# Kernel optimization log

Measured on AMD Instinct MI355X. Metric: run time of the kernel, lower is better.

## Reference

```python
import jax, jax.numpy as jnp
import numpy as np

EPS = 1e-5


def conv2d(x, w, b, stride=1, pad=1):
    out = jax.lax.conv_general_dilated(
        x, w, (stride, stride), [(pad, pad), (pad, pad)],
        dimension_numbers=('NCHW', 'OIHW', 'NCHW'))
    return out + b[None, :, None, None]


def bn_inf(x, gamma, beta, mean, var):
    inv = gamma / jnp.sqrt(var + EPS)
    return x * inv[None, :, None, None] + (beta - mean * inv)[None, :, None, None]


def deform_conv(x, offset, weight, stride, pad, dil):
    # x: [B,Ci,H,W], offset: [B,2*K*K,Ho,Wo] (dy,dx interleaved per kernel pos),
    # weight: [Co,Ci,K,K]. torchvision DeformConv2d v1 semantics, no bias.
    B, Ci, H, W = x.shape
    Co, _, K, _ = weight.shape
    KK = K * K
    Ho = (H + 2 * pad - dil * (K - 1) - 1) // stride + 1
    Wo = (W + 2 * pad - dil * (K - 1) - 1) // stride + 1
    dy = offset[:, 0::2]  # [B,KK,Ho,Wo]
    dx = offset[:, 1::2]
    ky, kx = jnp.meshgrid(jnp.arange(K), jnp.arange(K), indexing='ij')
    ky = ky.reshape(KK).astype(x.dtype)
    kx = kx.reshape(KK).astype(x.dtype)
    base_y = (jnp.arange(Ho) * stride - pad).astype(x.dtype)
    base_x = (jnp.arange(Wo) * stride - pad).astype(x.dtype)
    ys = base_y[None, None, :, None] + (ky * dil)[None, :, None, None] + dy
    xs = base_x[None, None, None, :] + (kx * dil)[None, :, None, None] + dx
    y0 = jnp.floor(ys)
    x0 = jnp.floor(xs)
    fy = ys - y0
    fx = xs - x0

    def gather(img, iy, ix):
        # img: [Ci,H,W]; iy, ix: [KK,Ho,Wo] float integer-valued coords
        valid = (iy >= 0) & (iy < H) & (ix >= 0) & (ix < W)
        iyc = jnp.clip(iy, 0, H - 1).astype(jnp.int32)
        ixc = jnp.clip(ix, 0, W - 1).astype(jnp.int32)
        v = img[:, iyc, ixc]  # [Ci,KK,Ho,Wo]
        return v * valid[None].astype(img.dtype)

    def sample_one(img, y0b, x0b, fyb, fxb):
        w00 = (1 - fyb) * (1 - fxb)
        w01 = (1 - fyb) * fxb
        w10 = fyb * (1 - fxb)
        w11 = fyb * fxb
        s = (gather(img, y0b, x0b) * w00[None]
             + gather(img, y0b, x0b + 1) * w01[None]
             + gather(img, y0b + 1, x0b) * w10[None]
             + gather(img, y0b + 1, x0b + 1) * w11[None])
        return s  # [Ci,KK,Ho,Wo]

    sampled = jax.vmap(sample_one)(x, y0, x0, fy, fx)  # [B,Ci,KK,Ho,Wo]
    return jnp.einsum('oik,bikhw->bohw', weight.reshape(Co, Ci, KK), sampled)


def setup_inputs() -> dict:
    key = jax.random.key(0)
    ks = jax.random.split(key, 16)
    B, C, H, W = 8, 128, 64, 64
    d = dict(
        x=jax.random.normal(ks[0], (B, C, H, W), jnp.float32),
        w_off1=jax.random.normal(ks[1], (18, C, 3, 3), jnp.float32) * 0.01,
        b_off1=jnp.zeros((18,), jnp.float32),
        w_dc1=jax.random.normal(ks[2], (C, C, 3, 3), jnp.float32) * 0.05,
        g1=jnp.ones((C,), jnp.float32),
        beta1=jnp.zeros((C,), jnp.float32),
        m1=jax.random.normal(ks[3], (C,), jnp.float32) * 0.1,
        v1=jax.random.uniform(ks[4], (C,), jnp.float32) + 0.5,
        w_off2=jax.random.normal(ks[5], (18, C, 3, 3), jnp.float32) * 0.01,
        b_off2=jnp.zeros((18,), jnp.float32),
        w_dc2=jax.random.normal(ks[6], (C, C, 3, 3), jnp.float32) * 0.05,
        g2=jnp.ones((C,), jnp.float32),
        beta2=jnp.zeros((C,), jnp.float32),
        m2=jax.random.normal(ks[7], (C,), jnp.float32) * 0.1,
        v2=jax.random.uniform(ks[8], (C,), jnp.float32) + 0.5,
    )
    return d


def reference(x, w_off1, b_off1, w_dc1, g1, beta1, m1, v1,
              w_off2, b_off2, w_dc2, g2, beta2, m2, v2):
    # BasicBlock6 forward (stride=1, in_planes==planes => identity shortcut)
    off1 = conv2d(x, w_off1, b_off1, stride=1, pad=1)
    out = jax.nn.relu(bn_inf(deform_conv(x, off1, w_dc1, 1, 2, 2), g1, beta1, m1, v1))
    off2 = conv2d(out, w_off2, b_off2, stride=1, pad=1)
    out = bn_inf(deform_conv(out, off2, w_dc2, 1, 2, 2), g2, beta2, m2, v2)
    out = out + x  # identity shortcut
    return jax.nn.relu(out)
```

## Files before the change

kernel.cpp:

```cpp
#include <hip/hip_runtime.h>
#include <hip/hip_bf16.h>

#define CH   128
#define HH   64
#define WW   64
#define OFFC 18

typedef __attribute__((ext_vector_type(8))) short bf16x8;
typedef __attribute__((ext_vector_type(4))) short bf16x4;
typedef __attribute__((ext_vector_type(4))) float f32x4;

static __device__ __forceinline__ unsigned short f2bf(float f) {
    __hip_bfloat16 h = __float2bfloat16(f);
    return *reinterpret_cast<unsigned short*>(&h);
}
static __device__ __forceinline__ float bf2f(unsigned short u) {
    union { unsigned int i; float f; } x; x.i = ((unsigned int)u) << 16;
    return x.f;
}

__global__ __launch_bounds__(256) void prep_kernel(
    const float* __restrict__ x, unsigned short* __restrict__ xh,
    const float* __restrict__ wdc1, const float* __restrict__ wdc2,
    const float* __restrict__ wof1, const float* __restrict__ wof2,
    unsigned short* __restrict__ wpk1, unsigned short* __restrict__ wpk2,
    unsigned short* __restrict__ wpo1, unsigned short* __restrict__ wpo2)
{
    __shared__ float s[CH][WW + 1];
    int blk = blockIdx.x;
    int tid = threadIdx.x;

    if (blk < 1152) {
        const float* w = (blk < 576) ? wdc1 : wdc2;
        unsigned short* wp = (blk < 576) ? wpk1 : wpk2;
        int id = (blk % 576) * 256 + tid;
        int j    = id & 7;
        int lane = (id >> 3) & 63;
        int ot   = (id >> 9) & 7;
        int kk   = (id >> 12) & 3;
        int k    = id >> 14;
        int o = ot * 16 + (lane & 15);
        int i = kk * 32 + (lane >> 4) * 8 + j;
        wp[id] = f2bf(w[(o * CH + i) * 9 + k]);
        return;
    }
    if (blk < 1440) {
        const float* w = (blk < 1296) ? wof1 : wof2;
        unsigned short* wp = (blk < 1296) ? wpo1 : wpo2;
        int id = ((blk - 1152) % 144) * 256 + tid;
        int j    = id & 7;
        int lane = (id >> 3) & 63;
        int mt   = (id >> 9) & 1;
        int kk   = (id >> 10) & 3;
        int k    = id >> 12;
        int o = mt * 16 + (lane & 15);
        int i = kk * 32 + (lane >> 4) * 8 + j;
        wp[id] = (o < OFFC) ? f2bf(w[(o * CH + i) * 9 + k]) : (unsigned short)0;
        return;
    }

    int nb = blk - 1440;
    const float* xb = x + ((size_t)(nb >> 6) * CH * HH + (nb & 63)) * WW;

    int c_off = tid >> 4, w0 = (tid & 15) * 4;
    #pragma unroll
    for (int it = 0; it < 8; ++it) {
        int c = it * 16 + c_off;
        float4 vv = *(const float4*)&xb[(size_t)c * HH * WW + w0];
        s[c][w0] = vv.x; s[c][w0 + 1] = vv.y; s[c][w0 + 2] = vv.z; s[c][w0 + 3] = vv.w;
    }
    __syncthreads();

    int w = tid & 63, c0 = (tid >> 6) * 32;
    unsigned short* dst = xh + ((size_t)nb * WW + w) * CH + c0;
    unsigned short tmp[32];
    #pragma unroll
    for (int j = 0; j < 32; ++j) tmp[j] = f2bf(s[c0 + j][w]);
    #pragma unroll
    for (int q = 0; q < 4; ++q)
        *(bf16x8*)(dst + q * 8) = *(const bf16x8*)(tmp + q * 8);
}

__global__ __launch_bounds__(256) void off_conv_mfma_kernel(
    const unsigned short* __restrict__ xh,
    const unsigned short* __restrict__ wpo,
    const float* __restrict__ bias,
    unsigned short* __restrict__ offh)
{
    int wgid = blockIdx.x;
    int blk  = (wgid & 7) * 64 + (wgid >> 3);
    int b = blk >> 6, oh = blk & 63;
    int tid = threadIdx.x;
    int lane = tid & 63;
    int nt = tid >> 6;
    int nl = lane & 15;
    int kg = lane >> 4;

    f32x4 acc0 = {0.f, 0.f, 0.f, 0.f}, acc1 = {0.f, 0.f, 0.f, 0.f};
    const unsigned short* xb = xh + (size_t)b * HH * WW * CH;

    for (int k = 0; k < 9; ++k) {
        int ky = k / 3, kx = k - ky * 3;
        int ih = oh - 1 + ky;
        if (ih < 0 || ih >= HH) continue;
        int iw = nt * 16 + nl + kx - 1;
        bool valid = (iw >= 0) && (iw < WW);
        const unsigned short* row = xb + ((size_t)ih * WW + (valid ? iw : 0)) * CH + kg * 8;
        const unsigned short* wk = wpo + (size_t)k * 8 * 512;
        #pragma unroll
        for (int kk = 0; kk < 4; ++kk) {
            bf16x8 bfrag = {0, 0, 0, 0, 0, 0, 0, 0};
            if (valid) bfrag = *(const bf16x8*)(row + kk * 32);
            bf16x8 a0 = *(const bf16x8*)(wk + (kk * 2 + 0) * 512 + lane * 8);
            bf16x8 a1 = *(const bf16x8*)(wk + (kk * 2 + 1) * 512 + lane * 8);
            acc0 = __builtin_amdgcn_mfma_f32_16x16x32_bf16(a0, bfrag, acc0, 0, 0, 0);
            acc1 = __builtin_amdgcn_mfma_f32_16x16x32_bf16(a1, bfrag, acc1, 0, 0, 0);
        }
    }

    int ow = nt * 16 + nl;
    #pragma unroll
    for (int r = 0; r < 4; ++r) {
        int co = kg * 4 + r;
        offh[(((size_t)b * OFFC + co) * HH + oh) * WW + ow] = f2bf(acc0[r] + bias[co]);
    }
    if (kg == 0) {
        #pragma unroll
        for (int r = 0; r < 2; ++r) {
            int co = 16 + r;
            offh[(((size_t)b * OFFC + co) * HH + oh) * WW + ow] = f2bf(acc1[r] + bias[co]);
        }
    }
}

#define DEF_COORD(K) do {                                                     \
    int ky = (K) / 3, kx = (K) - ky * 3;                                      \
    float ys = (float)(oh - 2 + ky * 2) + dyv[K];                             \
    float xs = (float)(ow_g - 2 + kx * 2) + dxv[K];                           \
    float y0f = floorf(ys), x0f = floorf(xs);                                 \
    float fy = ys - y0f, fx = xs - x0f;                                       \
    int y0 = (int)y0f, x0i = (int)x0f;                                        \
    int y1 = y0 + 1, x1 = x0i + 1;                                            \
    bool vy0 = (y0 >= 0) & (y0 < HH), vy1 = (y1 >= 0) & (y1 < HH);            \
    bool vx0 = (x0i >= 0) & (x0i < WW), vx1 = (x1 >= 0) & (x1 < WW);          \
    int y0c = min(max(y0, 0), HH - 1), y1c = min(max(y1, 0), HH - 1);         \
    int x0c = min(max(x0i, 0), WW - 1), x1c = min(max(x1, 0), WW - 1);        \
    cw0 = (1.f - fy) * (1.f - fx) * ((vy0 && vx0) ? 1.f : 0.f);               \
    cw1 = (1.f - fy) * fx         * ((vy0 && vx1) ? 1.f : 0.f);               \
    cw2 = fy * (1.f - fx)         * ((vy1 && vx0) ? 1.f : 0.f);               \
    cw3 = fy * fx                 * ((vy1 && vx1) ? 1.f : 0.f);               \
    p0 = xb + ((size_t)(y0c * WW + x0c)) * CH + ci0;                          \
    p1 = xb + ((size_t)(y0c * WW + x1c)) * CH + ci0;                          \
    p2 = xb + ((size_t)(y1c * WW + x0c)) * CH + ci0;                          \
    p3 = xb + ((size_t)(y1c * WW + x1c)) * CH + ci0;                          \
} while (0)

#define DEF_LOADS() do {                                                      \
    s0a = *(const bf16x8*)(p0); s0b = *(const bf16x8*)(p0 + 8);               \
    s1a = *(const bf16x8*)(p1); s1b = *(const bf16x8*)(p1 + 8);               \
    s2a = *(const bf16x8*)(p2); s2b = *(const bf16x8*)(p2 + 8);               \
    s3a = *(const bf16x8*)(p3); s3b = *(const bf16x8*)(p3 + 8);               \
} while (0)

#define DEF_BLEND_WRITE(BUF) do {                                             \
    union { bf16x8 v8; unsigned short u[8]; } w0u, w1u;                       \
    _Pragma("unroll")                                                         \
    for (int j = 0; j < 8; ++j) {                                             \
        float a0 = cw0 * bf2f((unsigned short)s0a[j])                         \
                 + cw1 * bf2f((unsigned short)s1a[j])                         \
                 + cw2 * bf2f((unsigned short)s2a[j])                         \
                 + cw3 * bf2f((unsigned short)s3a[j]);                        \
        float a1 = cw0 * bf2f((unsigned short)s0b[j])                         \
                 + cw1 * bf2f((unsigned short)s1b[j])                         \
                 + cw2 * bf2f((unsigned short)s2b[j])                         \
                 + cw3 * bf2f((unsigned short)s3b[j]);                        \
        w0u.u[j] = f2bf(a0); w1u.u[j] = f2bf(a1);                             \
    }                                                                         \
    int base = s_ow * 256 + ci0 * 2;                                          \
    int swz  = (s_ow & 7) << 4;                                               \
    *(bf16x8*)((char*)sB[BUF] + ( base        ^ swz)) = w0u.v8;               \
    *(bf16x8*)((char*)sB[BUF] + ((base + 16)  ^ swz)) = w1u.v8;               \
} while (0)

#define DEF_MFMA(K, BUF) do {                                                 \
    const unsigned short* wk = wpk + (size_t)(K) * 16384;                     \
    _Pragma("unroll")                                                         \
    for (int kk = 0; kk < 4; ++kk) {                                          \
        bf16x8 a0 = *(const bf16x8*)(wk + (kk * 8 + 2 * wv)     * 512 + lane * 8); \
        bf16x8 a1 = *(const bf16x8*)(wk + (kk * 8 + 2 * wv + 1) * 512 + lane * 8); \
        _Pragma("unroll")                                                     \
        for (int owt = 0; owt < 2; ++owt) {                                   \
            int owl = owt * 16 + (lane & 15);                                 \
            int rbyte = (owl * 256 + (kk * 32 + (lane >> 4) * 8) * 2)         \
                        ^ ((owl & 7) << 4);                                   \
            bf16x8 bfv = *(const bf16x8*)((const char*)sB[BUF] + rbyte);      \
            acc[0][owt] = __builtin_amdgcn_mfma_f32_16x16x32_bf16(            \
                              a0, bfv, acc[0][owt], 0, 0, 0);                 \
            acc[1][owt] = __builtin_amdgcn_mfma_f32_16x16x32_bf16(            \
                              a1, bfv, acc[1][owt], 0, 0, 0);                 \
        }                                                                     \
    }                                                                         \
} while (0)

__global__ __launch_bounds__(256) void deform_mfma2_kernel(
    const unsigned short* __restrict__ xh,
    const unsigned short* __restrict__ offh,
    const unsigned short* __restrict__ wpk,
    const float* __restrict__ g, const float* __restrict__ beta,
    const float* __restrict__ m, const float* __restrict__ v,
    const float* __restrict__ residual,
    unsigned short* __restrict__ out_h,
    float* __restrict__ out_f)
{
    __shared__ unsigned short sB[2][32 * 128];

    int wgid = blockIdx.x;
    int blk  = (wgid & 7) * 128 + (wgid >> 3);
    int owh = blk & 1, oh = (blk >> 1) & 63, b = blk >> 7;
    int ow0 = owh * 32;
    int tid = threadIdx.x, lane = tid & 63, wv = tid >> 6;

    int s_ow = tid >> 3;
    int ci0  = (tid & 7) * 16;
    int ow_g = ow0 + s_ow;

    const unsigned short* xb = xh + (size_t)b * HH * WW * CH;

    float dyv[9], dxv[9];
    #pragma unroll
    for (int k = 0; k < 9; ++k) {
        dyv[k] = bf2f(offh[(((size_t)b * OFFC + 2 * k)     * HH + oh) * WW + ow_g]);
        dxv[k] = bf2f(offh[(((size_t)b * OFFC + 2 * k + 1) * HH + oh) * WW + ow_g]);
    }

    f32x4 acc[2][2];
    #pragma unroll
    for (int a = 0; a < 2; ++a)
        #pragma unroll
        for (int q = 0; q < 2; ++q) acc[a][q] = (f32x4){0.f, 0.f, 0.f, 0.f};

    float cw0, cw1, cw2, cw3;
    const unsigned short *p0, *p1, *p2, *p3;
    bf16x8 s0a, s0b, s1a, s1b, s2a, s2b, s3a, s3b;

    DEF_COORD(0); DEF_LOADS(); DEF_BLEND_WRITE(0);
    __syncthreads();

    #pragma unroll
    for (int k = 0; k < 9; ++k) {
        if (k < 8) { DEF_COORD(k + 1); DEF_LOADS(); }
        DEF_MFMA(k, k & 1);
        if (k < 8) DEF_BLEND_WRITE((k + 1) & 1);
        __syncthreads();
    }

    if (out_h != nullptr) {
        #pragma unroll
        for (int otl = 0; otl < 2; ++otl) {
            int ob = (2 * wv + otl) * 16 + (lane >> 4) * 4;
            float inv[4], sh[4];
            #pragma unroll
            for (int r = 0; r < 4; ++r) {
                int o = ob + r;
                float iv = g[o] / sqrtf(v[o] + 1e-5f);
                inv[r] = iv; sh[r] = beta[o] - m[o] * iv;
            }
            #pragma unroll
            for (int owt = 0; owt < 2; ++owt) {
                int ow = ow0 + owt * 16 + (lane & 15);
                union { bf16x4 v4; unsigned short u[4]; } pk;
                #pragma unroll
                for (int r = 0; r < 4; ++r) {
                    float val = acc[otl][owt][r] * inv[r] + sh[r];
                    pk.u[r] = f2bf(fmaxf(val, 0.f));
                }
                *(bf16x4*)(out_h + ((size_t)(b * HH + oh) * WW + ow) * CH + ob) = pk.v4;
            }
        }
    } else {
        #pragma unroll
        for (int otl = 0; otl < 2; ++otl) {
            #pragma unroll
            for (int r = 0; r < 4; ++r) {
                int o = (2 * wv + otl) * 16 + (lane >> 4) * 4 + r;
                float iv = g[o] / sqrtf(v[o] + 1e-5f);
                float sh = beta[o] - m[o] * iv;
                #pragma unroll
                for (int owt = 0; owt < 2; ++owt) {
                    int ow = ow0 + owt * 16 + (lane & 15);
                    size_t idx = (((size_t)b * CH + o) * HH + oh) * WW + ow;
                    float val = acc[otl][owt][r] * iv + sh + residual[idx];
                    out_f[idx] = fmaxf(val, 0.f);
                }
            }
        }
    }
}

extern "C" void kernel_launch(void* const* d_in, const int* in_sizes, int n_in,
                              void* d_out, int out_size, void* d_ws, size_t ws_size,
                              hipStream_t stream)
{
    const float* x      = (const float*)d_in[0];
    const float* w_off1 = (const float*)d_in[1];
    const float* b_off1 = (const float*)d_in[2];
    const float* w_dc1  = (const float*)d_in[3];
    const float* g1     = (const float*)d_in[4];
    const float* beta1  = (const float*)d_in[5];
    const float* m1     = (const float*)d_in[6];
    const float* v1     = (const float*)d_in[7];
    const float* w_off2 = (const float*)d_in[8];
    const float* b_off2 = (const float*)d_in[9];
    const float* w_dc2  = (const float*)d_in[10];
    const float* g2     = (const float*)d_in[11];
    const float* beta2  = (const float*)d_in[12];
    const float* m2     = (const float*)d_in[13];
    const float* v2     = (const float*)d_in[14];
    float* out = (float*)d_out;

    char* ws = (char*)d_ws;
    unsigned short* xh    = (unsigned short*)ws;
    unsigned short* out1h = (unsigned short*)(ws + 8388608);
    unsigned short* offh  = (unsigned short*)(ws + 16777216);
    unsigned short* wpk1  = (unsigned short*)(ws + 17956864);
    unsigned short* wpk2  = (unsigned short*)(ws + 18251776);
    unsigned short* wpo1  = (unsigned short*)(ws + 18546688);
    unsigned short* wpo2  = (unsigned short*)(ws + 18620416);

    prep_kernel<<<1952, 256, 0, stream>>>(x, xh, w_dc1, w_dc2, w_off1, w_off2,
                                          wpk1, wpk2, wpo1, wpo2);

    off_conv_mfma_kernel<<<512, 256, 0, stream>>>(xh, wpo1, b_off1, offh);
    deform_mfma2_kernel<<<1024, 256, 0, stream>>>(xh, offh, wpk1,
                                                  g1, beta1, m1, v1,
                                                  nullptr, out1h, nullptr);
    off_conv_mfma_kernel<<<512, 256, 0, stream>>>(out1h, wpo2, b_off2, offh);
    deform_mfma2_kernel<<<1024, 256, 0, stream>>>(out1h, offh, wpk2,
                                                  g2, beta2, m2, v2,
                                                  x, nullptr, out);
}
```

Measured before the change: 102.8 us.

## Prefetch MFMA weight fragments into registers and single-buffer LDS tile

The deformable conv kernel now loads the next kernel position's weight A-fragments into a double-buffered register array while MFMAs consume the current one, instead of loading weights inline before each MFMA. The LDS B tile is reduced from double to single buffer, which adds an extra barrier per step between the MFMA reads and the blend write. The launch bounds now request 2 workgroups per CU. The goal is to hide global weight-load latency and raise occupancy, at the cost of more registers for the prefetched fragments and an extra synchronisation per step.

```diff
diff --git a/kernel.cpp b/kernel.cpp
--- a/kernel.cpp
+++ b/kernel.cpp
@@ -106,7 +106,7 @@
         int iw = nt * 16 + nl + kx - 1;
         bool valid = (iw >= 0) && (iw < WW);
         const unsigned short* row = xb + ((size_t)ih * WW + (valid ? iw : 0)) * CH + kg * 8;
-        const unsigned short* wk = wpo + (size_t)k * 8 * 512;
+        const unsigned short* wk = wpo + (size_t)k * 4096;
         #pragma unroll
         for (int kk = 0; kk < 4; ++kk) {
             bf16x8 bfrag = {0, 0, 0, 0, 0, 0, 0, 0};
@@ -155,14 +155,23 @@
     p3 = xb + ((size_t)(y1c * WW + x1c)) * CH + ci0;                          \
 } while (0)
 
-#define DEF_LOADS() do {                                                      \
+#define DEF_GATHER() do {                                                     \
     s0a = *(const bf16x8*)(p0); s0b = *(const bf16x8*)(p0 + 8);               \
     s1a = *(const bf16x8*)(p1); s1b = *(const bf16x8*)(p1 + 8);               \
     s2a = *(const bf16x8*)(p2); s2b = *(const bf16x8*)(p2 + 8);               \
     s3a = *(const bf16x8*)(p3); s3b = *(const bf16x8*)(p3 + 8);               \
 } while (0)
 
-#define DEF_BLEND_WRITE(BUF) do {                                             \
+#define DEF_ALOADS(K, ARR) do {                                               \
+    const unsigned short* wk_ = wpk + (size_t)(K) * 16384;                    \
+    _Pragma("unroll")                                                         \
+    for (int kk = 0; kk < 4; ++kk) {                                          \
+        ARR[kk * 2 + 0] = *(const bf16x8*)(wk_ + (kk * 8 + 2 * wv)     * 512 + lane * 8); \
+        ARR[kk * 2 + 1] = *(const bf16x8*)(wk_ + (kk * 8 + 2 * wv + 1) * 512 + lane * 8); \
+    }                                                                         \
+} while (0)
+
+#define DEF_BLEND_WRITE() do {                                                \
     union { bf16x8 v8; unsigned short u[8]; } w0u, w1u;                       \
     _Pragma("unroll")                                                         \
     for (int j = 0; j < 8; ++j) {                                             \
@@ -176,33 +185,38 @@
                  + cw3 * bf2f((unsigned short)s3b[j]);                        \
         w0u.u[j] = f2bf(a0); w1u.u[j] = f2bf(a1);                             \
     }                                                                         \
-    int base = s_ow * 256 + ci0 * 2;                                          \
-    int swz  = (s_ow & 7) << 4;                                               \
-    *(bf16x8*)((char*)sB[BUF] + ( base        ^ swz)) = w0u.v8;               \
-    *(bf16x8*)((char*)sB[BUF] + ((base + 16)  ^ swz)) = w1u.v8;               \
-} while (0)
-
-#define DEF_MFMA(K, BUF) do {                                                 \
-    const unsigned short* wk = wpk + (size_t)(K) * 16384;                     \
+    int base_ = s_ow * 256 + ci0 * 2;                                         \
+    int swz_  = (s_ow & 7) << 4;                                              \
+    *(bf16x8*)((char*)sB + ( base_        ^ swz_)) = w0u.v8;                  \
+    *(bf16x8*)((char*)sB + ((base_ + 16)  ^ swz_)) = w1u.v8;                  \
+} while (0)
+
+#define DEF_MFMA(ARR) do {                                                    \
     _Pragma("unroll")                                                         \
     for (int kk = 0; kk < 4; ++kk) {                                          \
-        bf16x8 a0 = *(const bf16x8*)(wk + (kk * 8 + 2 * wv)     * 512 + lane * 8); \
-        bf16x8 a1 = *(const bf16x8*)(wk + (kk * 8 + 2 * wv + 1) * 512 + lane * 8); \
         _Pragma("unroll")                                                     \
         for (int owt = 0; owt < 2; ++owt) {                                   \
             int owl = owt * 16 + (lane & 15);                                 \
             int rbyte = (owl * 256 + (kk * 32 + (lane >> 4) * 8) * 2)         \
                         ^ ((owl & 7) << 4);                                   \
-            bf16x8 bfv = *(const bf16x8*)((const char*)sB[BUF] + rbyte);      \
+            bf16x8 bfv = *(const bf16x8*)((const char*)sB + rbyte);           \
             acc[0][owt] = __builtin_amdgcn_mfma_f32_16x16x32_bf16(            \
-                              a0, bfv, acc[0][owt], 0, 0, 0);                 \
+                              ARR[kk * 2 + 0], bfv, acc[0][owt], 0, 0, 0);    \
             acc[1][owt] = __builtin_amdgcn_mfma_f32_16x16x32_bf16(            \
-                              a1, bfv, acc[1][owt], 0, 0, 0);                 \
+                              ARR[kk * 2 + 1], bfv, acc[1][owt], 0, 0, 0);    \
         }                                                                     \
     }                                                                         \
 } while (0)
 
-__global__ __launch_bounds__(256) void deform_mfma2_kernel(
+#define DEF_STEP(KN, ARRN, ARRC) do {                                         \
+    DEF_COORD(KN); DEF_GATHER(); DEF_ALOADS(KN, ARRN);                        \
+    DEF_MFMA(ARRC);                                                           \
+    __syncthreads();                                                          \
+    DEF_BLEND_WRITE();                                                        \
+    __syncthreads();                                                          \
+} while (0)
+
+__global__ __launch_bounds__(256, 2) void deform_mfma2_kernel(
     const unsigned short* __restrict__ xh,
     const unsigned short* __restrict__ offh,
     const unsigned short* __restrict__ wpk,
@@ -212,7 +226,7 @@
     unsigned short* __restrict__ out_h,
     float* __restrict__ out_f)
 {
-    __shared__ unsigned short sB[2][32 * 128];
+    __shared__ unsigned short sB[32 * 128];
 
     int wgid = blockIdx.x;
     int blk  = (wgid & 7) * 128 + (wgid >> 3);
@@ -242,17 +256,21 @@
     float cw0, cw1, cw2, cw3;
     const unsigned short *p0, *p1, *p2, *p3;
     bf16x8 s0a, s0b, s1a, s1b, s2a, s2b, s3a, s3b;
-
-    DEF_COORD(0); DEF_LOADS(); DEF_BLEND_WRITE(0);
+    bf16x8 aA[8], aB[8];
+
+    DEF_COORD(0); DEF_GATHER(); DEF_ALOADS(0, aA);
+    DEF_BLEND_WRITE();
     __syncthreads();
 
-    #pragma unroll
-    for (int k = 0; k < 9; ++k) {
-        if (k < 8) { DEF_COORD(k + 1); DEF_LOADS(); }
-        DEF_MFMA(k, k & 1);
-        if (k < 8) DEF_BLEND_WRITE((k + 1) & 1);
-        __syncthreads();
-    }
+    DEF_STEP(1, aB, aA);
+    DEF_STEP(2, aA, aB);
+    DEF_STEP(3, aB, aA);
+    DEF_STEP(4, aA, aB);
+    DEF_STEP(5, aB, aA);
+    DEF_STEP(6, aA, aB);
+    DEF_STEP(7, aB, aA);
+    DEF_STEP(8, aA, aB);
+    DEF_MFMA(aA);
 
     if (out_h != nullptr) {
         #pragma unroll
```

After: 96.67 us. -6.0%, faster.
